# Kernel tuning notes

Measured on AMD Instinct MI355X. Metric: run time of the kernel, lower is better.

Reference implementation:

```python
import jax, jax.numpy as jnp
import numpy as np

D = 256; NH = 8; NLEV = 4; NPTS = 4; DH = D // NH
DFFN = 1024; B = 8; LQ = 900
SHAPES = np.array([[100, 100], [50, 50], [25, 25], [13, 13]], dtype=np.int64)
STARTS = np.concatenate([[0], np.cumsum(SHAPES[:, 0] * SHAPES[:, 1])[:-1]]).astype(np.int64)
LEN = int((SHAPES[:, 0] * SHAPES[:, 1]).sum())


def _ln(x, w, b, eps=1e-5):
    m = x.mean(-1, keepdims=True)
    v = ((x - m) ** 2).mean(-1, keepdims=True)
    return (x - m) / jnp.sqrt(v + eps) * w + b


def _msdeform(q, ref, src, val_w, val_b, off_w, off_b, aw_w, aw_b, op_w, op_b):
    # Multi-scale deformable attention (Deformable DETR core), grid_sample
    # bilinear / zeros padding / align_corners=False semantics.
    Bq, Lq = q.shape[0], q.shape[1]
    value = (src @ val_w + val_b).reshape(Bq, -1, NH, DH)
    off = (q @ off_w + off_b).reshape(Bq, Lq, NH, NLEV, NPTS, 2)
    aw = jax.nn.softmax((q @ aw_w + aw_b).reshape(Bq, Lq, NH, NLEV * NPTS), -1)
    aw = aw.reshape(Bq, Lq, NH, NLEV, NPTS)
    norm = jnp.asarray(SHAPES[:, ::-1].copy(), dtype=q.dtype)  # (W_l, H_l)
    loc = ref[:, :, None, :, None, :] + off / norm[None, None, None, :, None, :]
    out = jnp.zeros((Bq, Lq, NH, DH), q.dtype)
    for l in range(NLEV):
        Hl, Wl = int(SHAPES[l, 0]), int(SHAPES[l, 1]); s = int(STARTS[l])
        v = value[:, s:s + Hl * Wl]                  # [B, Hl*Wl, NH, DH]
        lx = loc[:, :, :, l, :, 0] * Wl - 0.5        # align_corners=False pixel coords
        ly = loc[:, :, :, l, :, 1] * Hl - 0.5        # [B, Lq, NH, NPTS]
        x0 = jnp.floor(lx); y0 = jnp.floor(ly)
        fx = lx - x0; fy = ly - y0
        x0 = x0.astype(jnp.int32); y0 = y0.astype(jnp.int32)
        samp = jnp.zeros((Bq, Lq, NH, NPTS, DH), q.dtype)
        for dx, dy in ((0, 0), (1, 0), (0, 1), (1, 1)):
            xi = x0 + dx; yi = y0 + dy
            w = (fx if dx else 1.0 - fx) * (fy if dy else 1.0 - fy)
            valid = (xi >= 0) & (xi < Wl) & (yi >= 0) & (yi < Hl)
            idx = jnp.clip(yi, 0, Hl - 1) * Wl + jnp.clip(xi, 0, Wl - 1)
            idx_f = idx.transpose(0, 1, 3, 2).reshape(Bq, Lq * NPTS, NH)
            g = jnp.take_along_axis(v, idx_f[..., None], axis=1)
            g = g.reshape(Bq, Lq, NPTS, NH, DH).transpose(0, 1, 3, 2, 4)
            samp = samp + jnp.where(valid, w, 0.0)[..., None] * g
        out = out + jnp.sum(samp * aw[:, :, :, l, :, None], axis=3)
    return out.reshape(Bq, Lq, D) @ op_w + op_b


def _forward(tgt, query_pos, reference_points, src, qkv_w, qkv_b, out_w, out_b,
             ln2_w, ln2_b, val_w, val_b, off_w, off_b, aw_w, aw_b, op_w, op_b,
             ln1_w, ln1_b, w1, b1, w2, b2, ln3_w, ln3_b):
    Bq, Lq, _ = tgt.shape
    # --- self attention: q=k=tgt+pos, value=tgt (eval mode, no dropout) ---
    q = tgt + query_pos
    wq, wk, wv = qkv_w[:, :D], qkv_w[:, D:2 * D], qkv_w[:, 2 * D:]
    bq, bk, bv = qkv_b[:D], qkv_b[D:2 * D], qkv_b[2 * D:]
    qh = (q @ wq + bq).reshape(Bq, Lq, NH, DH)
    kh = (q @ wk + bk).reshape(Bq, Lq, NH, DH)
    vh = (tgt @ wv + bv).reshape(Bq, Lq, NH, DH)
    scores = jnp.einsum('bqhd,bkhd->bhqk', qh, kh) / jnp.sqrt(jnp.asarray(DH, tgt.dtype))
    attn = jax.nn.softmax(scores, -1)
    sa = jnp.einsum('bhqk,bkhd->bqhd', attn, vh).reshape(Bq, Lq, D) @ out_w + out_b
    tgt = _ln(tgt + sa, ln2_w, ln2_b)
    # --- multi-scale deformable cross attention ---
    ca = _msdeform(tgt + query_pos, reference_points, src,
                   val_w, val_b, off_w, off_b, aw_w, aw_b, op_w, op_b)
    tgt = _ln(tgt + ca, ln1_w, ln1_b)
    # --- FFN ---
    ff = jax.nn.relu(tgt @ w1 + b1) @ w2 + b2
    return _ln(tgt + ff, ln3_w, ln3_b)


def setup_inputs():
    key = jax.random.key(0)
    ks = jax.random.split(key, 16)
    s = 0.02
    return {
        'tgt': jax.random.normal(ks[0], (B, LQ, D), jnp.float32),
        'query_pos': jax.random.normal(ks[1], (B, LQ, D), jnp.float32),
        'reference_points': jax.random.uniform(ks[2], (B, LQ, NLEV, 2), jnp.float32),
        'src': jax.random.normal(ks[3], (B, LEN, D), jnp.float32),
        'spatial_shapes': jnp.asarray(SHAPES),
        'level_start_index': jnp.asarray(STARTS),
        'qkv_w': jax.random.normal(ks[4], (D, 3 * D), jnp.float32) * s,
        'qkv_b': jnp.zeros((3 * D,), jnp.float32),
        'out_w': jax.random.normal(ks[5], (D, D), jnp.float32) * s,
        'out_b': jnp.zeros((D,), jnp.float32),
        'ln2_w': jnp.ones((D,), jnp.float32), 'ln2_b': jnp.zeros((D,), jnp.float32),
        'val_w': jax.random.normal(ks[6], (D, D), jnp.float32) * s,
        'val_b': jnp.zeros((D,), jnp.float32),
        'off_w': jax.random.normal(ks[7], (D, NH * NLEV * NPTS * 2), jnp.float32) * s,
        'off_b': jax.random.normal(ks[8], (NH * NLEV * NPTS * 2,), jnp.float32) * 0.5,
        'aw_w': jax.random.normal(ks[9], (D, NH * NLEV * NPTS), jnp.float32) * s,
        'aw_b': jnp.zeros((NH * NLEV * NPTS,), jnp.float32),
        'op_w': jax.random.normal(ks[10], (D, D), jnp.float32) * s,
        'op_b': jnp.zeros((D,), jnp.float32),
        'ln1_w': jnp.ones((D,), jnp.float32), 'ln1_b': jnp.zeros((D,), jnp.float32),
        'w1': jax.random.normal(ks[11], (D, DFFN), jnp.float32) * s,
        'b1': jnp.zeros((DFFN,), jnp.float32),
        'w2': jax.random.normal(ks[12], (DFFN, D), jnp.float32) * s,
        'b2': jnp.zeros((D,), jnp.float32),
        'ln3_w': jnp.ones((D,), jnp.float32), 'ln3_b': jnp.zeros((D,), jnp.float32),
    }


def reference(tgt, query_pos, reference_points, src, spatial_shapes, level_start_index,
              qkv_w, qkv_b, out_w, out_b, ln2_w, ln2_b, val_w, val_b, off_w, off_b,
              aw_w, aw_b, op_w, op_b, ln1_w, ln1_b, w1, b1, w2, b2, ln3_w, ln3_b):
    return _forward(tgt, query_pos, reference_points, src, qkv_w, qkv_b, out_w, out_b,
                    ln2_w, ln2_b, val_w, val_b, off_w, off_b, aw_w, aw_b, op_w, op_b,
                    ln1_w, ln1_b, w1, b1, w2, b2, ln3_w, ln3_b)
```

## Files before the change

kernel.cpp:

```cpp
#include <hip/hip_runtime.h>
#include <math.h>

#define Dm    256
#define NHm   8
#define DHm   32
#define NLEVm 4
#define NPTSm 4
#define DFFNm 1024
#define Bm    8
#define LQm   900
#define LENm  13294
#define MQ    (Bm * LQm)
#define MV    (Bm * LENm)
#define MQP   7296
#define MVP   106368
#define LQP   960

typedef __attribute__((ext_vector_type(8))) short short8;
typedef __attribute__((ext_vector_type(4))) float f32x4;

__device__ __forceinline__ unsigned short f2bf(float f) {
    unsigned int b = __float_as_uint(f);
    unsigned int r = (b + 0x7FFFu + ((b >> 16) & 1u)) >> 16;
    return (unsigned short)r;
}
__device__ __forceinline__ float bf2f(unsigned short u) {
    return __uint_as_float(((unsigned int)u) << 16);
}

__global__ __launch_bounds__(256) void prep0(const float* __restrict__ tgt,
                                             const float* __restrict__ qpos,
                                             unsigned short* __restrict__ tgtb,
                                             unsigned short* __restrict__ qb,
                                             int n4, int n4pad) {
    int i = blockIdx.x * blockDim.x + threadIdx.x;
    int stride = gridDim.x * blockDim.x;
    for (; i < n4pad; i += stride) {
        ushort4 ut, uq;
        if (i < n4) {
            float4 x = reinterpret_cast<const float4*>(tgt)[i];
            float4 y = reinterpret_cast<const float4*>(qpos)[i];
            ut.x = f2bf(x.x); ut.y = f2bf(x.y); ut.z = f2bf(x.z); ut.w = f2bf(x.w);
            uq.x = f2bf(x.x + y.x); uq.y = f2bf(x.y + y.y);
            uq.z = f2bf(x.z + y.z); uq.w = f2bf(x.w + y.w);
        } else {
            ut.x = ut.y = ut.z = ut.w = 0;
            uq.x = uq.y = uq.z = uq.w = 0;
        }
        reinterpret_cast<ushort4*>(tgtb)[i] = ut;
        reinterpret_cast<ushort4*>(qb)[i] = uq;
    }
}

__global__ __launch_bounds__(256) void vtpad_kernel(unsigned short* __restrict__ vt) {
    int i = blockIdx.x * 256 + threadIdx.x;
    int row = i / 60, c = 900 + (i % 60);
    vt[(size_t)row * LQP + c] = 0;
}

__global__ __launch_bounds__(256) void wt_tiled(const float* __restrict__ W,
                                                unsigned short* __restrict__ BT,
                                                int N, int K) {
    __shared__ float tile[64][65];
    int n0 = blockIdx.x * 64, k0 = blockIdx.y * 64;
    int t = threadIdx.x;
    #pragma unroll
    for (int r0 = 0; r0 < 64; r0 += 16) {
        int r = r0 + (t >> 4);
        int c = (t & 15) * 4;
        float4 v = *reinterpret_cast<const float4*>(W + (size_t)(k0 + r) * N + n0 + c);
        tile[r][c + 0] = v.x; tile[r][c + 1] = v.y; tile[r][c + 2] = v.z; tile[r][c + 3] = v.w;
    }
    __syncthreads();
    #pragma unroll
    for (int s = t; s < 512; s += 256) {
        int r = s >> 3, c8 = (s & 7) * 8;
        short8 u;
        #pragma unroll
        for (int j = 0; j < 8; ++j) u[j] = (short)f2bf(tile[c8 + j][r]);
        *reinterpret_cast<short8*>(BT + (size_t)(n0 + r) * K + k0 + c8) = u;
    }
}

template <int RELU, int OBF>
__global__ __launch_bounds__(256) void bgemm(int M, int N, int K,
        const unsigned short* __restrict__ A,
        const unsigned short* __restrict__ BT,
        const float* __restrict__ bias, const float* __restrict__ bias2,
        float* __restrict__ Cf, float* __restrict__ Cf2,
        unsigned short* __restrict__ Cb, int ldc) {
    __shared__ __align__(16) unsigned short As[2][128 * 32];
    __shared__ __align__(16) unsigned short Bs[2][128 * 32];
    int t = threadIdx.x;
    int l = t & 63;
    int w = t >> 6;
    int row0 = blockIdx.x * 128, col0 = blockIdx.y * 128;
    int wr = (w >> 1) * 64, wc = (w & 1) * 64;
    f32x4 acc[4][4];
    #pragma unroll
    for (int m = 0; m < 4; ++m)
        #pragma unroll
        for (int n = 0; n < 4; ++n) acc[m][n] = (f32x4){0.f, 0.f, 0.f, 0.f};

    int s0 = t, s1 = t + 256;
    const unsigned short* Ag = A + (size_t)row0 * K;
    const unsigned short* Bg = BT + (size_t)col0 * K;
    const unsigned short* a0p = Ag + (size_t)(s0 >> 2) * K + (s0 & 3) * 8;
    const unsigned short* a1p = Ag + (size_t)(s1 >> 2) * K + (s1 & 3) * 8;
    const unsigned short* b0p = Bg + (size_t)(s0 >> 2) * K + (s0 & 3) * 8;
    const unsigned short* b1p = Bg + (size_t)(s1 >> 2) * K + (s1 & 3) * 8;

    short8 ra0 = *(const short8*)(a0p);
    short8 ra1 = *(const short8*)(a1p);
    short8 rb0 = *(const short8*)(b0p);
    short8 rb1 = *(const short8*)(b1p);

    int cur = 0;
    for (int k0 = 0; k0 < K; k0 += 32) {
        unsigned short* Ac = As[cur];
        unsigned short* Bc = Bs[cur];
        *(short8*)(Ac + s0 * 8) = ra0;
        *(short8*)(Ac + s1 * 8) = ra1;
        *(short8*)(Bc + s0 * 8) = rb0;
        *(short8*)(Bc + s1 * 8) = rb1;
        if (k0 + 32 < K) {
            ra0 = *(const short8*)(a0p + k0 + 32);
            ra1 = *(const short8*)(a1p + k0 + 32);
            rb0 = *(const short8*)(b0p + k0 + 32);
            rb1 = *(const short8*)(b1p + k0 + 32);
        }
        __syncthreads();
        short8 af[4], bfr[4];
        #pragma unroll
        for (int m = 0; m < 4; ++m)
            af[m] = *(const short8*)(Ac + (wr + m * 16 + (l & 15)) * 32 + (l >> 4) * 8);
        #pragma unroll
        for (int n = 0; n < 4; ++n)
            bfr[n] = *(const short8*)(Bc + (wc + n * 16 + (l & 15)) * 32 + (l >> 4) * 8);
        #pragma unroll
        for (int m = 0; m < 4; ++m)
            #pragma unroll
            for (int n = 0; n < 4; ++n)
                acc[m][n] = __builtin_amdgcn_mfma_f32_16x16x32_bf16(af[m], bfr[n], acc[m][n], 0, 0, 0);
        cur ^= 1;
    }

    int cr = (l >> 4) * 4;
    int cc = l & 15;
    #pragma unroll
    for (int m = 0; m < 4; ++m) {
        #pragma unroll
        for (int n = 0; n < 4; ++n) {
            int col = col0 + wc + n * 16 + cc;
            if (OBF == 2) {
                float bv = bias[col];
                int r0 = row0 + wr + m * 16 + cr;
                if (r0 < M) {
                    int bb = r0 / 900;
                    int q = r0 - bb * 900;
                    ushort4 u;
                    u.x = f2bf(acc[m][n][0] + bv);
                    u.y = f2bf(acc[m][n][1] + bv);
                    u.z = f2bf(acc[m][n][2] + bv);
                    u.w = f2bf(acc[m][n][3] + bv);
                    *reinterpret_cast<ushort4*>(Cb + ((size_t)(bb * 256 + col)) * LQP + q) = u;
                }
            } else if (OBF == 3) {
                float bv = (col < 256) ? bias[col] : bias2[col - 256];
                #pragma unroll
                for (int j = 0; j < 4; ++j) {
                    int r = row0 + wr + m * 16 + cr + j;
                    if (r < M) {
                        float v = acc[m][n][j] + bv;
                        if (col < 256) Cf[(size_t)r * 256 + col] = v;
                        else           Cf2[(size_t)r * 128 + (col - 256)] = v;
                    }
                }
            } else {
                float bv = bias[col];
                #pragma unroll
                for (int j = 0; j < 4; ++j) {
                    int r = row0 + wr + m * 16 + cr + j;
                    if (r < M) {
                        float v = acc[m][n][j] + bv;
                        if (RELU) v = fmaxf(v, 0.f);
                        if (OBF) Cb[(size_t)r * ldc + col] = f2bf(v);
                        else     Cf[(size_t)r * ldc + col] = v;
                    }
                }
            }
        }
    }
}

__global__ __launch_bounds__(256) void bgemm_vf(int M, int N, int K,
        const float* __restrict__ A,
        const unsigned short* __restrict__ BT,
        const float* __restrict__ bias,
        unsigned short* __restrict__ Cb, int ldc) {
    __shared__ __align__(16) unsigned short As[2][128 * 32];
    __shared__ __align__(16) unsigned short Bs[2][128 * 32];
    int t = threadIdx.x;
    int l = t & 63;
    int w = t >> 6;
    int row0 = blockIdx.x * 128, col0 = blockIdx.y * 128;
    int wr = (w >> 1) * 64, wc = (w & 1) * 64;
    f32x4 acc[4][4];
    #pragma unroll
    for (int m = 0; m < 4; ++m)
        #pragma unroll
        for (int n = 0; n < 4; ++n) acc[m][n] = (f32x4){0.f, 0.f, 0.f, 0.f};

    int s0 = t, s1 = t + 256;
    int r0c = min(row0 + (s0 >> 2), M - 1);
    int r1c = min(row0 + (s1 >> 2), M - 1);
    const float* a0p = A + (size_t)r0c * K + (s0 & 3) * 8;
    const float* a1p = A + (size_t)r1c * K + (s1 & 3) * 8;
    const unsigned short* Bg = BT + (size_t)col0 * K;
    const unsigned short* b0p = Bg + (size_t)(s0 >> 2) * K + (s0 & 3) * 8;
    const unsigned short* b1p = Bg + (size_t)(s1 >> 2) * K + (s1 & 3) * 8;

    float4 fa0 = *(const float4*)(a0p);
    float4 fa1 = *(const float4*)(a0p + 4);
    float4 fb0 = *(const float4*)(a1p);
    float4 fb1 = *(const float4*)(a1p + 4);
    short8 rb0 = *(const short8*)(b0p);
    short8 rb1 = *(const short8*)(b1p);

    int cur = 0;
    for (int k0 = 0; k0 < K; k0 += 32) {
        unsigned short* Ac = As[cur];
        unsigned short* Bc = Bs[cur];
        short8 ra0, ra1;
        ra0[0] = (short)f2bf(fa0.x); ra0[1] = (short)f2bf(fa0.y);
        ra0[2] = (short)f2bf(fa0.z); ra0[3] = (short)f2bf(fa0.w);
        ra0[4] = (short)f2bf(fa1.x); ra0[5] = (short)f2bf(fa1.y);
        ra0[6] = (short)f2bf(fa1.z); ra0[7] = (short)f2bf(fa1.w);
        ra1[0] = (short)f2bf(fb0.x); ra1[1] = (short)f2bf(fb0.y);
        ra1[2] = (short)f2bf(fb0.z); ra1[3] = (short)f2bf(fb0.w);
        ra1[4] = (short)f2bf(fb1.x); ra1[5] = (short)f2bf(fb1.y);
        ra1[6] = (short)f2bf(fb1.z); ra1[7] = (short)f2bf(fb1.w);
        *(short8*)(Ac + s0 * 8) = ra0;
        *(short8*)(Ac + s1 * 8) = ra1;
        *(short8*)(Bc + s0 * 8) = rb0;
        *(short8*)(Bc + s1 * 8) = rb1;
        if (k0 + 32 < K) {
            fa0 = *(const float4*)(a0p + k0 + 32);
            fa1 = *(const float4*)(a0p + k0 + 36);
            fb0 = *(const float4*)(a1p + k0 + 32);
            fb1 = *(const float4*)(a1p + k0 + 36);
            rb0 = *(const short8*)(b0p + k0 + 32);
            rb1 = *(const short8*)(b1p + k0 + 32);
        }
        __syncthreads();
        short8 af[4], bfr[4];
        #pragma unroll
        for (int m = 0; m < 4; ++m)
            af[m] = *(const short8*)(Ac + (wr + m * 16 + (l & 15)) * 32 + (l >> 4) * 8);
        #pragma unroll
        for (int n = 0; n < 4; ++n)
            bfr[n] = *(const short8*)(Bc + (wc + n * 16 + (l & 15)) * 32 + (l >> 4) * 8);
        #pragma unroll
        for (int m = 0; m < 4; ++m)
            #pragma unroll
            for (int n = 0; n < 4; ++n)
                acc[m][n] = __builtin_amdgcn_mfma_f32_16x16x32_bf16(af[m], bfr[n], acc[m][n], 0, 0, 0);
        cur ^= 1;
    }

    int cr = (l >> 4) * 4;
    int cc = l & 15;
    #pragma unroll
    for (int m = 0; m < 4; ++m) {
        #pragma unroll
        for (int n = 0; n < 4; ++n) {
            int col = col0 + wc + n * 16 + cc;
            float bv = bias[col];
            #pragma unroll
            for (int j = 0; j < 4; ++j) {
                int r = row0 + wr + m * 16 + cr + j;
                if (r < M)
                    Cb[(size_t)r * ldc + col] = f2bf(acc[m][n][j] + bv);
            }
        }
    }
}

__global__ __launch_bounds__(256) void flash_mfma(const unsigned short* __restrict__ qk,
                                                  const unsigned short* __restrict__ vt,
                                                  unsigned short* __restrict__ out) {
    __shared__ unsigned short P_lds[4][16][72];
    int t = threadIdx.x;
    int l = t & 63, w = t >> 6;
    int lr = l & 15, lg = l >> 4;
    int qt = blockIdx.x, h = blockIdx.y, b = blockIdx.z;
    const float scale = 0.17677669529663687f;

    short8 qf = *(const short8*)(qk + (size_t)(b * LQm + qt * 64 + w * 16 + lr) * 512 + h * 32 + lg * 8);

    f32x4 accO[2];
    accO[0] = (f32x4){0.f, 0.f, 0.f, 0.f};
    accO[1] = (f32x4){0.f, 0.f, 0.f, 0.f};
    float mrow[4] = {-1e30f, -1e30f, -1e30f, -1e30f};
    float lrow[4] = {0.f, 0.f, 0.f, 0.f};
    const f32x4 zero = (f32x4){0.f, 0.f, 0.f, 0.f};
    const unsigned short* vtb = vt + ((size_t)(b * 256 + h * 32)) * LQP;

    for (int kt = 0; kt < 15; ++kt) {
        int k0 = kt * 64;
        f32x4 sfr[4];
        #pragma unroll
        for (int ks = 0; ks < 4; ++ks) {
            short8 kf = *(const short8*)(qk + (size_t)(b * LQm + k0 + ks * 16 + lr) * 512 + 256 + h * 32 + lg * 8);
            sfr[ks] = __builtin_amdgcn_mfma_f32_16x16x32_bf16(qf, kf, zero, 0, 0, 0);
        }
        float sv[4][4];
        #pragma unroll
        for (int ks = 0; ks < 4; ++ks) {
            bool valid = (k0 + ks * 16 + lr) < LQm;
            #pragma unroll
            for (int j = 0; j < 4; ++j)
                sv[ks][j] = valid ? sfr[ks][j] * scale : -1e30f;
        }
        float tm[4], newm[4], rr[4], ps[4];
        #pragma unroll
        for (int j = 0; j < 4; ++j)
            tm[j] = fmaxf(fmaxf(sv[0][j], sv[1][j]), fmaxf(sv[2][j], sv[3][j]));
        #pragma unroll
        for (int msk = 1; msk <= 8; msk <<= 1) {
            #pragma unroll
            for (int j = 0; j < 4; ++j) tm[j] = fmaxf(tm[j], __shfl_xor(tm[j], msk));
        }
        #pragma unroll
        for (int j = 0; j < 4; ++j) {
            newm[j] = fmaxf(mrow[j], tm[j]);
            rr[j] = __expf(mrow[j] - newm[j]);
            mrow[j] = newm[j];
            ps[j] = 0.f;
        }
        float pv[4][4];
        #pragma unroll
        for (int ks = 0; ks < 4; ++ks)
            #pragma unroll
            for (int j = 0; j < 4; ++j) {
                pv[ks][j] = __expf(sv[ks][j] - newm[j]);
                ps[j] += pv[ks][j];
            }
        #pragma unroll
        for (int msk = 1; msk <= 8; msk <<= 1) {
            #pragma unroll
            for (int j = 0; j < 4; ++j) ps[j] += __shfl_xor(ps[j], msk);
        }
        #pragma unroll
        for (int j = 0; j < 4; ++j) lrow[j] = lrow[j] * rr[j] + ps[j];
        #pragma unroll
        for (int n = 0; n < 2; ++n)
            #pragma unroll
            for (int j = 0; j < 4; ++j) accO[n][j] *= rr[j];
        #pragma unroll
        for (int ks = 0; ks < 4; ++ks)
            #pragma unroll
            for (int j = 0; j < 4; ++j)
                P_lds[w][lg * 4 + j][ks * 16 + lr] = f2bf(pv[ks][j]);
        #pragma unroll
        for (int kh2 = 0; kh2 < 2; ++kh2) {
            short8 pf = *(const short8*)(&P_lds[w][lr][kh2 * 32 + lg * 8]);
            #pragma unroll
            for (int n = 0; n < 2; ++n) {
                short8 vf = *(const short8*)(vtb + (size_t)(n * 16 + lr) * LQP + k0 + kh2 * 32 + lg * 8);
                accO[n] = __builtin_amdgcn_mfma_f32_16x16x32_bf16(pf, vf, accO[n], 0, 0, 0);
            }
        }
    }
    float inv[4];
    #pragma unroll
    for (int j = 0; j < 4; ++j) inv[j] = 1.0f / lrow[j];
    #pragma unroll
    for (int n = 0; n < 2; ++n)
        #pragma unroll
        for (int j = 0; j < 4; ++j) {
            int q = qt * 64 + w * 16 + lg * 4 + j;
            if (q < LQm)
                out[(size_t)(b * LQm + q) * 256 + h * 32 + n * 16 + lr] = f2bf(accO[n][j] * inv[j]);
        }
}

template <int DUAL, int QP>
__global__ __launch_bounds__(256) void add_ln_kernel(const float* __restrict__ x,
                                                     const float* __restrict__ r,
                                                     const float* __restrict__ w,
                                                     const float* __restrict__ b,
                                                     const float* __restrict__ qpos,
                                                     float* __restrict__ out,
                                                     unsigned short* __restrict__ outb,
                                                     unsigned short* __restrict__ outq) {
    int row = blockIdx.x * 4 + (threadIdx.x >> 6);
    int lane = threadIdx.x & 63;
    size_t i4 = (size_t)row * 64 + lane;
    float4 xv = reinterpret_cast<const float4*>(x)[i4];
    float4 rv = reinterpret_cast<const float4*>(r)[i4];
    float4 v = make_float4(xv.x + rv.x, xv.y + rv.y, xv.z + rv.z, xv.w + rv.w);
    float s = v.x + v.y + v.z + v.w;
    #pragma unroll
    for (int msk = 1; msk <= 32; msk <<= 1) s += __shfl_xor(s, msk);
    float mean = s * (1.0f / Dm);
    float4 dv = make_float4(v.x - mean, v.y - mean, v.z - mean, v.w - mean);
    float sq = dv.x * dv.x + dv.y * dv.y + dv.z * dv.z + dv.w * dv.w;
    #pragma unroll
    for (int msk = 1; msk <= 32; msk <<= 1) sq += __shfl_xor(sq, msk);
    float is = rsqrtf(sq * (1.0f / Dm) + 1e-5f);
    float4 wv = reinterpret_cast<const float4*>(w)[lane];
    float4 bv = reinterpret_cast<const float4*>(b)[lane];
    float4 res = make_float4(dv.x * is * wv.x + bv.x, dv.y * is * wv.y + bv.y,
                             dv.z * is * wv.z + bv.z, dv.w * is * wv.w + bv.w);
    reinterpret_cast<float4*>(out)[i4] = res;
    if (DUAL) {
        ushort4 u;
        u.x = f2bf(res.x); u.y = f2bf(res.y); u.z = f2bf(res.z); u.w = f2bf(res.w);
        reinterpret_cast<ushort4*>(outb)[i4] = u;
    }
    if (QP) {
        float4 qv = reinterpret_cast<const float4*>(qpos)[i4];
        ushort4 u;
        u.x = f2bf(res.x + qv.x); u.y = f2bf(res.y + qv.y);
        u.z = f2bf(res.z + qv.z); u.w = f2bf(res.w + qv.w);
        reinterpret_cast<ushort4*>(outq)[i4] = u;
    }
}

__global__ __launch_bounds__(256) void msdeform_kernel(const unsigned short* __restrict__ value,
                                                       const float* __restrict__ ref,
                                                       const float* __restrict__ off,
                                                       const float* __restrict__ awl,
                                                       unsigned short* __restrict__ out) {
    const int HL[4] = {100, 50, 25, 13};
    const int ST[4] = {0, 10000, 12500, 13125};
    __shared__ float lsx[4][128], lsy[4][128], wtab[4][128];
    __shared__ float2 ctab[4][512];
    int wv = threadIdx.x >> 6, lane = threadIdx.x & 63;
    int m = blockIdx.x * 4 + wv;
    int b = m / LQm;

    #pragma unroll
    for (int e = lane; e < 128; e += 64) {
        int lev = (e >> 2) & 3;
        float rx = ref[((size_t)m * NLEVm + lev) * 2 + 0];
        float ry = ref[((size_t)m * NLEVm + lev) * 2 + 1];
        float ox = off[(size_t)m * 256 + e * 2 + 0];
        float oy = off[(size_t)m * 256 + e * 2 + 1];
        float Wf = (float)HL[lev];
        lsx[wv][e] = (rx + ox / Wf) * Wf - 0.5f;
        lsy[wv][e] = (ry + oy / Wf) * Wf - 0.5f;
        wtab[wv][e] = awl[(size_t)m * 128 + e];
    }
    __syncthreads();
    if (lane < NHm) {
        int h = lane;
        float mx = -1e30f;
        #pragma unroll
        for (int i = 0; i < 16; i++) mx = fmaxf(mx, wtab[wv][h * 16 + i]);
        float s = 0.f;
        #pragma unroll
        for (int i = 0; i < 16; i++) {
            float e = __expf(wtab[wv][h * 16 + i] - mx);
            wtab[wv][h * 16 + i] = e; s += e;
        }
        float inv = 1.0f / s;
        #pragma unroll
        for (int i = 0; i < 16; i++) wtab[wv][h * 16 + i] *= inv;
    }
    __syncthreads();
    #pragma unroll
    for (int j = 0; j < 8; ++j) {
        int e2 = lane * 8 + j;
        int c = e2 & 3, e = e2 >> 2;
        int lev = (e >> 2) & 3;
        int Wl = HL[lev];
        float lx = lsx[wv][e], ly = lsy[wv][e];
        float x0f = floorf(lx), y0f = floorf(ly);
        float fx = lx - x0f, fy = ly - y0f;
        int dx = c & 1, dy = c >> 1;
        int xi = (int)x0f + dx, yi = (int)y0f + dy;
        bool valid = (xi >= 0) && (xi < Wl) && (yi >= 0) && (yi < Wl);
        float wc = valid ? ((dx ? fx : 1.0f - fx) * (dy ? fy : 1.0f - fy)) * wtab[wv][e] : 0.f;
        int xc = min(max(xi, 0), Wl - 1), yc = min(max(yi, 0), Wl - 1);
        int row = b * LENm + ST[lev] + yc * Wl + xc;
        ctab[wv][e2] = make_float2(__int_as_float(row), wc);
    }
    __syncthreads();
    int h = lane >> 3, dg = lane & 7;
    const unsigned short* basep = value + h * 32 + dg * 4;
    float a0 = 0.f, a1 = 0.f, a2 = 0.f, a3 = 0.f;
    #pragma unroll
    for (int i = 0; i < 16; ++i) {
        #pragma unroll
        for (int c = 0; c < 4; ++c) {
            float2 cc = ctab[wv][(h * 16 + i) * 4 + c];
            int row = __float_as_int(cc.x);
            float wc = cc.y;
            ushort4 v = *reinterpret_cast<const ushort4*>(basep + (size_t)row * 256);
            a0 += wc * bf2f(v.x); a1 += wc * bf2f(v.y);
            a2 += wc * bf2f(v.z); a3 += wc * bf2f(v.w);
        }
    }
    ushort4 o;
    o.x = f2bf(a0); o.y = f2bf(a1); o.z = f2bf(a2); o.w = f2bf(a3);
    *reinterpret_cast<ushort4*>(out + (size_t)m * 256 + h * 32 + dg * 4) = o;
}

extern "C" void kernel_launch(void* const* d_in, const int* in_sizes, int n_in,
                              void* d_out, int out_size, void* d_ws, size_t ws_size,
                              hipStream_t stream) {
    const float* tgt   = (const float*)d_in[0];
    const float* qpos  = (const float*)d_in[1];
    const float* refp  = (const float*)d_in[2];
    const float* src   = (const float*)d_in[3];
    const float* qkv_w = (const float*)d_in[6];
    const float* qkv_b = (const float*)d_in[7];
    const float* out_w = (const float*)d_in[8];
    const float* out_b = (const float*)d_in[9];
    const float* ln2_w = (const float*)d_in[10];
    const float* ln2_b = (const float*)d_in[11];
    const float* val_w = (const float*)d_in[12];
    const float* val_b = (const float*)d_in[13];
    const float* off_w = (const float*)d_in[14];
    const float* off_b = (const float*)d_in[15];
    const float* aw_w  = (const float*)d_in[16];
    const float* aw_b  = (const float*)d_in[17];
    const float* op_w  = (const float*)d_in[18];
    const float* op_b  = (const float*)d_in[19];
    const float* ln1_w = (const float*)d_in[20];
    const float* ln1_b = (const float*)d_in[21];
    const float* w1    = (const float*)d_in[22];
    const float* b1    = (const float*)d_in[23];
    const float* w2    = (const float*)d_in[24];
    const float* b2    = (const float*)d_in[25];
    const float* ln3_w = (const float*)d_in[26];
    const float* ln3_b = (const float*)d_in[27];

    char* base = (char*)d_ws;
    unsigned short* value_bf  = (unsigned short*)(base);
    unsigned short* hidden_bf = (unsigned short*)(base + 54460416);
    unsigned short* t2_bf     = (unsigned short*)(base + 54460416 + 14942208);
    unsigned short* qk_bf = (unsigned short*)(base + 108920832);
    float* offb = (float*)(base + 108920832);
    float* awb  = (float*)(base + 108920832 + 7372800);
    unsigned short* Vt = (unsigned short*)(base + 123666432);
    float* S1   = (float*)(base + 123666432);
    float* t1   = (float*)(base + 131039232);
    float* t2   = (float*)(base + 138412032);
    unsigned short* Qbf     = (unsigned short*)(base + 145784832);
    unsigned short* tgt_bf  = (unsigned short*)(base + 149520384);
    unsigned short* attn_bf = (unsigned short*)(base + 153255936);
    unsigned short* ca_bf   = (unsigned short*)(base + 156991488);
    unsigned short* BT_qkv  = (unsigned short*)(base + 160727040);
    unsigned short* BT_out  = BT_qkv + 768 * 256;
    unsigned short* BT_val  = BT_out + 256 * 256;
    unsigned short* BT_off  = BT_val + 256 * 256;
    unsigned short* BT_aw   = BT_off + 256 * 256;
    unsigned short* BT_op   = BT_aw + 128 * 256;
    unsigned short* BT_w1   = BT_op + 256 * 256;
    unsigned short* BT_w2   = BT_w1 + 1024 * 256;
    float* outp = (float*)d_out;

    dim3 blk(256);
    wt_tiled<<<dim3(12, 4), blk, 0, stream>>>(qkv_w, BT_qkv, 768, 256);
    wt_tiled<<<dim3(4, 4),  blk, 0, stream>>>(out_w, BT_out, 256, 256);
    wt_tiled<<<dim3(4, 4),  blk, 0, stream>>>(val_w, BT_val, 256, 256);
    wt_tiled<<<dim3(4, 4),  blk, 0, stream>>>(off_w, BT_off, 256, 256);
    wt_tiled<<<dim3(2, 4),  blk, 0, stream>>>(aw_w,  BT_aw,  128, 256);
    wt_tiled<<<dim3(4, 4),  blk, 0, stream>>>(op_w,  BT_op,  256, 256);
    wt_tiled<<<dim3(16, 4), blk, 0, stream>>>(w1,    BT_w1, 1024, 256);
    wt_tiled<<<dim3(4, 16), blk, 0, stream>>>(w2,    BT_w2,  256, 1024);

    prep0<<<dim3(1824), blk, 0, stream>>>(tgt, qpos, tgt_bf, Qbf, MQ * Dm / 4, MQP * Dm / 4);

    bgemm<0, 1><<<dim3(57, 4), blk, 0, stream>>>(MQ, 512, 256, Qbf, BT_qkv, qkv_b, nullptr, nullptr, nullptr, qk_bf, 512);
    bgemm<0, 2><<<dim3(57, 2), blk, 0, stream>>>(MQ, 256, 256, tgt_bf, BT_qkv + 512 * 256, qkv_b + 512, nullptr, nullptr, nullptr, Vt, 256);
    vtpad_kernel<<<dim3(480), blk, 0, stream>>>(Vt);
    flash_mfma<<<dim3(15, NHm, Bm), blk, 0, stream>>>(qk_bf, Vt, attn_bf);
    bgemm<0, 0><<<dim3(57, 2), blk, 0, stream>>>(MQ, 256, 256, attn_bf, BT_out, out_b, nullptr, S1, nullptr, nullptr, 256);
    add_ln_kernel<0, 1><<<dim3(1800), blk, 0, stream>>>(tgt, S1, ln2_w, ln2_b, qpos, t1, nullptr, Qbf);
    bgemm_vf<<<dim3(831, 2), blk, 0, stream>>>(MV, 256, 256, src, BT_val, val_b, value_bf, 256);
    bgemm<0, 3><<<dim3(57, 3), blk, 0, stream>>>(MQ, 384, 256, Qbf, BT_off, off_b, aw_b, offb, awb, nullptr, 0);
    msdeform_kernel<<<dim3(1800), blk, 0, stream>>>(value_bf, refp, offb, awb, ca_bf);
    bgemm<0, 0><<<dim3(57, 2), blk, 0, stream>>>(MQ, 256, 256, ca_bf, BT_op, op_b, nullptr, S1, nullptr, nullptr, 256);
    add_ln_kernel<1, 0><<<dim3(1800), blk, 0, stream>>>(t1, S1, ln1_w, ln1_b, nullptr, t2, t2_bf, nullptr);
    bgemm<1, 1><<<dim3(57, 8), blk, 0, stream>>>(MQ, DFFNm, 256, t2_bf, BT_w1, b1, nullptr, nullptr, nullptr, hidden_bf, DFFNm);
    bgemm<0, 0><<<dim3(57, 2), blk, 0, stream>>>(MQ, 256, 1024, hidden_bf, BT_w2, b2, nullptr, S1, nullptr, nullptr, 256);
    add_ln_kernel<0, 0><<<dim3(1800), blk, 0, stream>>>(t2, S1, ln3_w, ln3_b, nullptr, outp, nullptr, nullptr);
}
```

Baseline: 281.5 us.

## Replace LDS-staged value projection GEMM with direct-load 64-row tile kernel

The value projection GEMM (src @ val_w, about 106k rows) drops LDS staging and double buffering. Each wave now loads its A fragments straight from global fp32 memory, converts them to bf16 in registers and feeds the MFMA, with all four waves sharing 64 rows and splitting the 256 output columns. This removes LDS traffic and the per-k-step syncthreads. In exchange, the 64-row strip of A is reread by all four waves, global loads are less coalesced, and there is no explicit prefetch.

```diff
diff --git a/kernel.cpp b/kernel.cpp
--- a/kernel.cpp
+++ b/kernel.cpp
@@ -193,94 +193,67 @@
     }
 }
 
-__global__ __launch_bounds__(256) void bgemm_vf(int M, int N, int K,
-        const float* __restrict__ A,
+__global__ __launch_bounds__(256) void bgemm_vd(const float* __restrict__ A,
         const unsigned short* __restrict__ BT,
         const float* __restrict__ bias,
-        unsigned short* __restrict__ Cb, int ldc) {
-    __shared__ __align__(16) unsigned short As[2][128 * 32];
-    __shared__ __align__(16) unsigned short Bs[2][128 * 32];
-    int t = threadIdx.x;
-    int l = t & 63;
-    int w = t >> 6;
-    int row0 = blockIdx.x * 128, col0 = blockIdx.y * 128;
-    int wr = (w >> 1) * 64, wc = (w & 1) * 64;
+        unsigned short* __restrict__ Cb) {
+    int l = threadIdx.x & 63, w = threadIdx.x >> 6;
+    int lr = l & 15, lg = l >> 4;
+    int row0 = blockIdx.x * 64;
+    int col0 = w * 64;
+
+    const float* ap[4];
+    #pragma unroll
+    for (int m = 0; m < 4; ++m) {
+        int r = min(row0 + m * 16 + lr, MV - 1);
+        ap[m] = A + (size_t)r * 256 + lg * 8;
+    }
+    const unsigned short* bp[4];
+    #pragma unroll
+    for (int n = 0; n < 4; ++n)
+        bp[n] = BT + (size_t)(col0 + n * 16 + lr) * 256 + lg * 8;
+
     f32x4 acc[4][4];
     #pragma unroll
     for (int m = 0; m < 4; ++m)
         #pragma unroll
         for (int n = 0; n < 4; ++n) acc[m][n] = (f32x4){0.f, 0.f, 0.f, 0.f};
 
-    int s0 = t, s1 = t + 256;
-    int r0c = min(row0 + (s0 >> 2), M - 1);
-    int r1c = min(row0 + (s1 >> 2), M - 1);
-    const float* a0p = A + (size_t)r0c * K + (s0 & 3) * 8;
-    const float* a1p = A + (size_t)r1c * K + (s1 & 3) * 8;
-    const unsigned short* Bg = BT + (size_t)col0 * K;
-    const unsigned short* b0p = Bg + (size_t)(s0 >> 2) * K + (s0 & 3) * 8;
-    const unsigned short* b1p = Bg + (size_t)(s1 >> 2) * K + (s1 & 3) * 8;
-
-    float4 fa0 = *(const float4*)(a0p);
-    float4 fa1 = *(const float4*)(a0p + 4);
-    float4 fb0 = *(const float4*)(a1p);
-    float4 fb1 = *(const float4*)(a1p + 4);
-    short8 rb0 = *(const short8*)(b0p);
-    short8 rb1 = *(const short8*)(b1p);
-
-    int cur = 0;
-    for (int k0 = 0; k0 < K; k0 += 32) {
-        unsigned short* Ac = As[cur];
-        unsigned short* Bc = Bs[cur];
-        short8 ra0, ra1;
-        ra0[0] = (short)f2bf(fa0.x); ra0[1] = (short)f2bf(fa0.y);
-        ra0[2] = (short)f2bf(fa0.z); ra0[3] = (short)f2bf(fa0.w);
-        ra0[4] = (short)f2bf(fa1.x); ra0[5] = (short)f2bf(fa1.y);
-        ra0[6] = (short)f2bf(fa1.z); ra0[7] = (short)f2bf(fa1.w);
-        ra1[0] = (short)f2bf(fb0.x); ra1[1] = (short)f2bf(fb0.y);
-        ra1[2] = (short)f2bf(fb0.z); ra1[3] = (short)f2bf(fb0.w);
-        ra1[4] = (short)f2bf(fb1.x); ra1[5] = (short)f2bf(fb1.y);
-        ra1[6] = (short)f2bf(fb1.z); ra1[7] = (short)f2bf(fb1.w);
-        *(short8*)(Ac + s0 * 8) = ra0;
-        *(short8*)(Ac + s1 * 8) = ra1;
-        *(short8*)(Bc + s0 * 8) = rb0;
-        *(short8*)(Bc + s1 * 8) = rb1;
-        if (k0 + 32 < K) {
-            fa0 = *(const float4*)(a0p + k0 + 32);
-            fa1 = *(const float4*)(a0p + k0 + 36);
-            fb0 = *(const float4*)(a1p + k0 + 32);
-            fb1 = *(const float4*)(a1p + k0 + 36);
-            rb0 = *(const short8*)(b0p + k0 + 32);
-            rb1 = *(const short8*)(b1p + k0 + 32);
-        }
-        __syncthreads();
+    #pragma unroll 2
+    for (int k0 = 0; k0 < 256; k0 += 32) {
         short8 af[4], bfr[4];
         #pragma unroll
-        for (int m = 0; m < 4; ++m)
-            af[m] = *(const short8*)(Ac + (wr + m * 16 + (l & 15)) * 32 + (l >> 4) * 8);
+        for (int m = 0; m < 4; ++m) {
+            float4 x0 = *(const float4*)(ap[m] + k0);
+            float4 x1 = *(const float4*)(ap[m] + k0 + 4);
+            af[m][0] = (short)f2bf(x0.x); af[m][1] = (short)f2bf(x0.y);
+            af[m][2] = (short)f2bf(x0.z); af[m][3] = (short)f2bf(x0.w);
+            af[m][4] = (short)f2bf(x1.x); af[m][5] = (short)f2bf(x1.y);
+            af[m][6] = (short)f2bf(x1.z); af[m][7] = (short)f2bf(x1.w);
+        }
         #pragma unroll
         for (int n = 0; n < 4; ++n)
-            bfr[n] = *(const short8*)(Bc + (wc + n * 16 + (l & 15)) * 32 + (l >> 4) * 8);
+            bfr[n] = *(const short8*)(bp[n] + k0);
         #pragma unroll
         for (int m = 0; m < 4; ++m)
             #pragma unroll
             for (int n = 0; n < 4; ++n)
                 acc[m][n] = __builtin_amdgcn_mfma_f32_16x16x32_bf16(af[m], bfr[n], acc[m][n], 0, 0, 0);
-        cur ^= 1;
-    }
-
-    int cr = (l >> 4) * 4;
-    int cc = l & 15;
+    }
+
+    int cr = lg * 4;
+    int cc = lr;
     #pragma unroll
     for (int m = 0; m < 4; ++m) {
         #pragma unroll
         for (int n = 0; n < 4; ++n) {
-            int col = col0 + wc + n * 16 + cc;
+            int col = col0 + n * 16 + cc;
             float bv = bias[col];
             #pragma unroll
             for (int j = 0; j < 4; ++j) {
-                int r = row0 + wr + m * 16 + cr + j;
-                if (r < M)
-                    Cb[(size_t)r * ldc + col] = f2bf(acc[m][n][j] + bv);
+                int r = row0 + m * 16 + cr + j;
+                if (r < MV)
+                    Cb[(size_t)r * 256 + col] = f2bf(acc[m][n][j] + bv);
             }
         }
     }
@@ -581,7 +554,7 @@
     flash_mfma<<<dim3(15, NHm, Bm), blk, 0, stream>>>(qk_bf, Vt, attn_bf);
     bgemm<0, 0><<<dim3(57, 2), blk, 0, stream>>>(MQ, 256, 256, attn_bf, BT_out, out_b, nullptr, S1, nullptr, nullptr, 256);
     add_ln_kernel<0, 1><<<dim3(1800), blk, 0, stream>>>(tgt, S1, ln2_w, ln2_b, qpos, t1, nullptr, Qbf);
-    bgemm_vf<<<dim3(831, 2), blk, 0, stream>>>(MV, 256, 256, src, BT_val, val_b, value_bf, 256);
+    bgemm_vd<<<dim3(1662), blk, 0, stream>>>(src, BT_val, val_b, value_bf);
     bgemm<0, 3><<<dim3(57, 3), blk, 0, stream>>>(MQ, 384, 256, Qbf, BT_off, off_b, aw_b, offb, awb, nullptr, 0);
     msdeform_kernel<<<dim3(1800), blk, 0, stream>>>(value_bf, refp, offb, awb, ca_bf);
     bgemm<0, 0><<<dim3(57, 2), blk, 0, stream>>>(MQ, 256, 256, ca_bf, BT_op, op_b, nullptr, S1, nullptr, nullptr, 256);
```

Result: slower. 331.9 us (+17.9%).
